# Kernel tuning notes

Hardware: AMD Instinct MI355X
Metric: run time of the kernel (lower is better)

## Reference

```python
import jax, jax.numpy as jnp
import numpy as np

N_CRYST = 256
ATOMS_PER = 64
N_ATOMS = N_CRYST * ATOMS_PER          # 16384
N_EDGES = N_ATOMS * 20                 # 327680 (max_neighbors=20)
HID = 128                              # hidden_dim / emb_size_atom / emb_size_edge
LAT = 256                              # latent_dim
NRAD = 128                             # radial basis size
NBLOCK = 3                             # interaction blocks
MAXZ = 100                             # MAX_ATOMIC_NUM
CUTOFF = 6.0


def lattice_matrix(lengths, angles):
    """CDVAE lattice_params_to_matrix: (B,3),(B,3 deg) -> (B,3,3)."""
    a, b, c = lengths[:, 0], lengths[:, 1], lengths[:, 2]
    al, be, ga = (jnp.deg2rad(angles[:, i]) for i in range(3))
    cos_a, cos_b, cos_g = jnp.cos(al), jnp.cos(be), jnp.cos(ga)
    sin_a, sin_b = jnp.sin(al), jnp.sin(be)
    val = jnp.clip((cos_a * cos_b - cos_g) / (sin_a * sin_b), -1.0, 1.0)
    gs = jnp.arccos(val)  # gamma*
    zero = jnp.zeros_like(a)
    va = jnp.stack([a * sin_b, zero, a * cos_b], -1)
    vb = jnp.stack([-b * sin_a * jnp.cos(gs), b * sin_a * jnp.sin(gs), b * cos_a], -1)
    vc = jnp.stack([zero, zero, c], -1)
    return jnp.stack([va, vb, vc], 1)


def setup_inputs() -> dict:
    key = jax.random.key(0)
    ks = jax.random.split(key, 20)
    p = lambda k, shp: jax.random.normal(k, shp, jnp.float32) * 0.05
    inp = {
        "z": jax.random.normal(ks[0], (N_CRYST, LAT), jnp.float32),
        "pred_frac_coords": jax.random.uniform(ks[1], (N_ATOMS, 3), jnp.float32),
        "pred_atom_types": jax.random.randint(ks[2], (N_ATOMS,), 0, MAXZ),
        "num_atoms": jnp.full((N_CRYST,), ATOMS_PER, jnp.int32),
        "lengths": 5.0 + 5.0 * jax.random.uniform(ks[3], (N_CRYST, 3), jnp.float32),
        "angles": 60.0 + 60.0 * jax.random.uniform(ks[4], (N_CRYST, 3), jnp.float32),
        "edge_index": jax.random.randint(ks[5], (2, N_EDGES), 0, N_ATOMS),
        # learned parameters
        "atom_emb": p(ks[6], (MAXZ, HID)),
        "W_in": p(ks[7], (HID + LAT, HID)), "b_in": jnp.zeros((HID,), jnp.float32),
        "W_rbf": p(ks[8], (NRAD, HID)),
        "W_edge": p(ks[9], (3 * HID, HID)), "b_edge": jnp.zeros((HID,), jnp.float32),
        "W_msg": p(ks[10], (NBLOCK, HID, HID)), "b_msg": jnp.zeros((NBLOCK, HID), jnp.float32),
        "W_gate": p(ks[11], (NBLOCK, HID, HID)),
        "W_upd": p(ks[12], (NBLOCK, HID, HID)), "b_upd": jnp.zeros((NBLOCK, HID), jnp.float32),
        "W_force": p(ks[13], (HID, 1)),
        "W_atom": p(ks[14], (HID, MAXZ)), "b_atom": jnp.zeros((MAXZ,), jnp.float32),
    }
    return inp


def reference(z, pred_frac_coords, pred_atom_types, num_atoms, lengths, angles,
              edge_index, atom_emb, W_in, b_in, W_rbf, W_edge, b_edge,
              W_msg, b_msg, W_gate, W_upd, b_upd, W_force, W_atom, b_atom):
    silu = jax.nn.silu
    batch = jnp.arange(N_ATOMS) // ATOMS_PER  # atom -> crystal (uniform 64 atoms/crystal)

    # fractional -> cartesian using per-crystal lattice
    latt = lattice_matrix(lengths, angles)                       # (B,3,3)
    cart = jnp.einsum("ni,nij->nj", pred_frac_coords, latt[batch])  # (N,3)

    src, dst = edge_index[0], edge_index[1]
    vec = cart[dst] - cart[src]                                   # (E,3)
    d = jnp.linalg.norm(vec, axis=-1) + 1e-8                      # (E,)
    unit = vec / d[:, None]

    # radial basis with smooth cosine envelope
    centers = jnp.linspace(0.0, CUTOFF, NRAD)
    width = CUTOFF / NRAD
    env = 0.5 * (jnp.cos(jnp.pi * jnp.clip(d / CUTOFF, 0.0, 1.0)) + 1.0)
    rbf = jnp.exp(-((d[:, None] - centers) ** 2) / (2.0 * width * width)) * env[:, None]
    rbf_h = rbf @ W_rbf                                           # (E,HID)

    # atom embedding conditioned on latent z (broadcast per crystal)
    h = silu(jnp.concatenate([atom_emb[pred_atom_types], z[batch]], -1) @ W_in + b_in)

    # edge embedding
    m = silu(jnp.concatenate([h[src], h[dst], rbf_h], -1) @ W_edge + b_edge)  # (E,HID)

    # interaction blocks: edge message update, rbf gating, scatter to atoms
    for i in range(NBLOCK):
        m2 = silu(m @ W_msg[i] + b_msg[i]) * (rbf_h @ W_gate[i])
        agg = jax.ops.segment_sum(m2, dst, num_segments=N_ATOMS)  # (N,HID)
        h = h + silu(agg @ W_upd[i] + b_upd[i])
        m = m + m2

    # per-edge force scalar -> cartesian coord diff per atom
    f_edge = (m @ W_force) * unit                                 # (E,3)
    pred_cart_coord_diff = jax.ops.segment_sum(f_edge, dst, num_segments=N_ATOMS)

    pred_atom_types_out = h @ W_atom + b_atom                     # (N,MAXZ)
    return (pred_cart_coord_diff, pred_atom_types_out)
```

## Files before the change

kernel.cpp:

```cpp
#include <hip/hip_runtime.h>
#include <hip/hip_bf16.h>

#define N_CRYST 256
#define ATOMS_PER 64
#define N_ATOMS (N_CRYST * ATOMS_PER)
#define N_EDGES (N_ATOMS * 20)
#define HID 128
#define LAT 256
#define NRAD 128
#define NBLOCK 3
#define MAXZ 100
#define CUTOFF 6.0f
#define PI_F 3.14159265358979323846f
#define ETILE 64
#define TABN 2048

typedef unsigned short ushort_t;
typedef unsigned char uchar_t;
typedef unsigned long long ull_t;
typedef __attribute__((ext_vector_type(8))) short short8;
typedef __attribute__((ext_vector_type(4))) float f32x4;

__device__ __forceinline__ float fexp2(float x) {
    float r; asm("v_exp_f32 %0, %1" : "=v"(r) : "v"(x)); return r;
}
__device__ __forceinline__ float frcp(float x) {
    float r; asm("v_rcp_f32 %0, %1" : "=v"(r) : "v"(x)); return r;
}
__device__ __forceinline__ float silu(float x) {
    return x * frcp(1.0f + fexp2(x * -1.44269504f));
}

__device__ __forceinline__ ushort_t f2bf(float v) {
    unsigned int u = __float_as_uint(v);
    return (ushort_t)((u + 0x7FFF + ((u >> 16) & 1)) >> 16);
}
__device__ __forceinline__ float bf2f(ushort_t u) {
    return __uint_as_float((unsigned int)u << 16);
}
__device__ __forceinline__ unsigned int pkbf(float lo, float hi) {
    unsigned int r;
    asm("v_cvt_pk_bf16_f32 %0, %1, %2" : "=v"(r) : "v"(lo), "v"(hi));
    return r;
}

__device__ __forceinline__ f32x4 MFMA(short8 a, short8 b, f32x4 c) {
    return __builtin_amdgcn_mfma_f32_16x16x32_bf16(a, b, c, 0, 0, 0);
}

__device__ __forceinline__ int swz(int row, int k) {
    return (row * 256 + k * 2) ^ ((row & 7) << 4);
}

__device__ __forceinline__ short8 ldB(const ushort_t* W, int col, int K, int k) {
    return *reinterpret_cast<const short8*>(W + (size_t)col * K + k);
}

__global__ void k_init(float* __restrict__ out, float* __restrict__ agg,
                       int* __restrict__ cnt) {
    int i = blockIdx.x * blockDim.x + threadIdx.x;
    if (i < N_ATOMS * 3) out[i] = 0.0f;
    if (i < N_ATOMS) cnt[i] = 0;
    if (i < NBLOCK * N_ATOMS * HID) agg[i] = 0.0f;
}

__global__ void k_hist(const int* __restrict__ edge_index, int* __restrict__ cnt) {
    int e = blockIdx.x * blockDim.x + threadIdx.x;
    if (e < N_EDGES) atomicAdd(&cnt[edge_index[N_EDGES + e]], 1);
}

__global__ void k_scan(const int* __restrict__ cnt, int* __restrict__ cursor) {
    __shared__ int partial[256];
    int t = threadIdx.x;
    int base = t * (N_ATOMS / 256);
    int s = 0;
    for (int j = 0; j < N_ATOMS / 256; j++) s += cnt[base + j];
    partial[t] = s;
    __syncthreads();
    if (t == 0) {
        int run = 0;
        for (int i = 0; i < 256; i++) { int v = partial[i]; partial[i] = run; run += v; }
    }
    __syncthreads();
    int run = partial[t];
    for (int j = 0; j < N_ATOMS / 256; j++) {
        cursor[base + j] = run;
        run += cnt[base + j];
    }
}

__global__ void k_scatter(const int* __restrict__ edge_index,
                          int* __restrict__ cursor, int* __restrict__ perm) {
    int e = blockIdx.x * blockDim.x + threadIdx.x;
    if (e < N_EDGES) {
        int pos = atomicAdd(&cursor[edge_index[N_EDGES + e]], 1);
        perm[pos] = e;
    }
}

__global__ void k_latt(const float* __restrict__ lengths,
                       const float* __restrict__ angles,
                       float* __restrict__ latt) {
    int c = blockIdx.x * blockDim.x + threadIdx.x;
    if (c >= N_CRYST) return;
    float a  = lengths[c * 3 + 0];
    float b  = lengths[c * 3 + 1];
    float cc = lengths[c * 3 + 2];
    float al = angles[c * 3 + 0] * (PI_F / 180.0f);
    float be = angles[c * 3 + 1] * (PI_F / 180.0f);
    float ga = angles[c * 3 + 2] * (PI_F / 180.0f);
    float cos_a = cosf(al), cos_b = cosf(be), cos_g = cosf(ga);
    float sin_a = sinf(al), sin_b = sinf(be);
    float val = (cos_a * cos_b - cos_g) / (sin_a * sin_b);
    val = fminf(1.0f, fmaxf(-1.0f, val));
    float gs = acosf(val);
    float* L = latt + c * 9;
    L[0] = a * sin_b;              L[1] = 0.0f;                  L[2] = a * cos_b;
    L[3] = -b * sin_a * cosf(gs);  L[4] = b * sin_a * sinf(gs);  L[5] = b * cos_a;
    L[6] = 0.0f;                   L[7] = 0.0f;                  L[8] = cc;
}

__global__ void k_cart(const float* __restrict__ frac,
                       const float* __restrict__ latt,
                       float* __restrict__ cart) {
    int n = blockIdx.x * blockDim.x + threadIdx.x;
    if (n >= N_ATOMS) return;
    int b = n / ATOMS_PER;
    const float* L = latt + b * 9;
    float f0 = frac[n * 3 + 0], f1 = frac[n * 3 + 1], f2 = frac[n * 3 + 2];
    cart[n * 3 + 0] = f0 * L[0] + f1 * L[3] + f2 * L[6];
    cart[n * 3 + 1] = f0 * L[1] + f1 * L[4] + f2 * L[7];
    cart[n * 3 + 2] = f0 * L[2] + f1 * L[5] + f2 * L[8];
}

__global__ void k_tab(const float* __restrict__ W_rbf, float* __restrict__ T) {
    int j = blockIdx.x;
    int c = threadIdx.x;
    __shared__ float rbf[NRAD];
    float d = (float)j * (CUTOFF / TABN);
    const float inv2w2 = 1.0f / (2.0f * (CUTOFF / NRAD) * (CUTOFF / NRAD));
    const float cstep = CUTOFF / (NRAD - 1);
    float x = fminf(1.0f, d * (1.0f / CUTOFF));
    float env = 0.5f * (cosf(PI_F * x) + 1.0f);
    float diff = d - (float)c * cstep;
    rbf[c] = expf(-diff * diff * inv2w2) * env;
    __syncthreads();
    float acc = 0.0f;
#pragma unroll 8
    for (int k = 0; k < NRAD; k++) acc += rbf[k] * W_rbf[k * HID + c];
    T[j * HID + c] = acc;
}

__global__ void k_prep(const float* __restrict__ W_edge,
                       const float* __restrict__ W_msg,
                       const float* __restrict__ W_gate,
                       const float* __restrict__ W_upd,
                       const float* __restrict__ W_atom,
                       ushort_t* __restrict__ Wt_edge,
                       ushort_t* __restrict__ Wt_msg,
                       ushort_t* __restrict__ Wt_gate,
                       ushort_t* __restrict__ Wt_upd,
                       ushort_t* __restrict__ Wt_atom) {
    int i = blockIdx.x * blockDim.x + threadIdx.x;
    if (i < 128 * 384) {
        int c = i / 384, k = i % 384;
        Wt_edge[(size_t)c * 384 + k] = f2bf(W_edge[k * 128 + c]);
    }
    if (i < 3 * 128 * 128) {
        int blk = i >> 14, r = i & 16383;
        int c = r >> 7, k = r & 127;
        Wt_msg[blk * 16384 + c * 128 + k]  = f2bf(W_msg[blk * 16384 + k * 128 + c]);
        Wt_gate[blk * 16384 + c * 128 + k] = f2bf(W_gate[blk * 16384 + k * 128 + c]);
        Wt_upd[blk * 16384 + c * 128 + k]  = f2bf(W_upd[blk * 16384 + k * 128 + c]);
    }
    if (i < 128 * 128) {
        int c = i >> 7, k = i & 127;
        Wt_atom[c * 128 + k] = (c < MAXZ) ? f2bf(W_atom[k * MAXZ + c]) : (ushort_t)0;
    }
}

__global__ void k_embW(const float* __restrict__ atom_emb,
                       const float* __restrict__ W_in,
                       const float* __restrict__ b_in,
                       float* __restrict__ embW) {
    int zi = blockIdx.x;
    int c = threadIdx.x;
    __shared__ float row[HID];
    row[c] = atom_emb[zi * HID + c];
    __syncthreads();
    float acc = b_in[c];
#pragma unroll 8
    for (int k = 0; k < HID; k++) acc += row[k] * W_in[k * HID + c];
    embW[zi * HID + c] = acc;
}

__global__ void k_zW(const float* __restrict__ z,
                     const float* __restrict__ W_in,
                     float* __restrict__ zW) {
    int b = blockIdx.x;
    int c = threadIdx.x;
    __shared__ float row[LAT];
    row[c]       = z[b * LAT + c];
    row[128 + c] = z[b * LAT + 128 + c];
    __syncthreads();
    float acc = 0.f;
#pragma unroll 8
    for (int k = 0; k < LAT; k++) acc += row[k] * W_in[(HID + k) * HID + c];
    zW[b * HID + c] = acc;
}

__global__ void k_h2(const int* __restrict__ types,
                     const float* __restrict__ embW,
                     const float* __restrict__ zW,
                     ushort_t* __restrict__ h_bf) {
    int idx = blockIdx.x * 256 + threadIdx.x;
    int n = idx >> 7, c = idx & 127;
    float v = embW[types[n] * HID + c] + zW[(n >> 6) * HID + c];
    h_bf[idx] = f2bf(silu(v));
}

__global__ __launch_bounds__(512, 4)
void k_edges(const int* __restrict__ perm,
             const int* __restrict__ edge_index,
             const float* __restrict__ cart,
             const float* __restrict__ T,
             const ushort_t* __restrict__ h_bf,
             const ushort_t* __restrict__ Wt_edge,
             const float* __restrict__ b_edge,
             const ushort_t* __restrict__ Wt_msg,
             const float* __restrict__ b_msg,
             const ushort_t* __restrict__ Wt_gate,
             const float* __restrict__ W_force,
             float* __restrict__ agg,
             float* __restrict__ outF)
{
    __shared__ ushort_t R2[ETILE * HID];
    __shared__ ushort_t HSR3[ETILE * HID];
    __shared__ ushort_t HD[ETILE * HID];
    __shared__ int   sm_dst[ETILE];
    __shared__ float sm_unit[ETILE][3];
    __shared__ float sm_d[ETILE];
    __shared__ float sm_f[ETILE];
    __shared__ uchar_t sm_runid8[ETILE];
    __shared__ int   sm_slotdst[ETILE];
    __shared__ int   sm_nruns;
    ushort_t* M2T = HD;

    const int t    = threadIdx.x;
    const int lane = t & 63;
    const int wave = t >> 6;
    const int l15  = lane & 15;
    const int g4   = lane >> 4;
    const int lk8  = 8 * g4;
    const int colw = wave * 16;
    const int e0   = blockIdx.x * ETILE;

    const int laneA = l15 * 256 + ((lk8 * 2) ^ ((l15 & 7) << 4));
    const int colM  = colw + l15;
    int woff[4];
#pragma unroll
    for (int r = 0; r < 4; r++) {
        int row = g4 * 4 + r;
        woff[r] = row * 256 + ((colM * 2) ^ ((row & 7) << 4));
    }

    if (t < ETILE) {
        int e = t;
        int eid = perm[e0 + e];
        int s = edge_index[eid];
        int d = edge_index[N_EDGES + eid];
        sm_dst[e] = d;
        float vx = cart[d * 3 + 0] - cart[s * 3 + 0];
        float vy = cart[d * 3 + 1] - cart[s * 3 + 1];
        float vz = cart[d * 3 + 2] - cart[s * 3 + 2];
        float dist = sqrtf(vx * vx + vy * vy + vz * vz) + 1e-8f;
        sm_d[e] = dist;
        float di = 1.0f / dist;
        sm_unit[e][0] = vx * di; sm_unit[e][1] = vy * di; sm_unit[e][2] = vz * di;
        sm_f[e] = 0.0f;
    }
    __syncthreads();

    short8 hs[2], hd[2];
    int stoff[2];
#pragma unroll
    for (int p = 0; p < 2; p++) {
        int u   = p * 512 + t;
        int row = u >> 4;
        int seg = u & 15;
        int eid = perm[e0 + row];
        int s = edge_index[eid];
        int d = edge_index[N_EDGES + eid];
        hs[p] = *reinterpret_cast<const short8*>(h_bf + (size_t)s * HID + seg * 8);
        hd[p] = *reinterpret_cast<const short8*>(h_bf + (size_t)d * HID + seg * 8);
        stoff[p] = swz(row, seg * 8);
    }

    if (wave == 0) {
        int e = lane;
        int d = sm_dst[e];
        int prev = (e == 0) ? -1 : sm_dst[e - 1];
        ull_t mask = __ballot(d != prev);
        int rid = __popcll(mask & ((2ull << e) - 1)) - 1;
        sm_runid8[e] = (uchar_t)rid;
        if (d != prev) sm_slotdst[rid] = d;
        if (e == 0) sm_nruns = __popcll(mask);
    }

    {
#pragma unroll
        for (int it = 0; it < 4; it++) {
            int u = it * 512 + t;
            int e = u >> 5;
            int p = u & 31;
            float idxf = sm_d[e] * (TABN / CUTOFF);
            idxf = fminf(idxf, (float)TABN);
            int j = (int)idxf;
            float fr = idxf - (float)j;
            f32x4 lo = *reinterpret_cast<const f32x4*>(T + (size_t)j * HID + 4 * p);
            f32x4 hi = *reinterpret_cast<const f32x4*>(T + (size_t)(j + 1) * HID + 4 * p);
            float v0 = lo[0] + fr * (hi[0] - lo[0]);
            float v1 = lo[1] + fr * (hi[1] - lo[1]);
            float v2 = lo[2] + fr * (hi[2] - lo[2]);
            float v3 = lo[3] + fr * (hi[3] - lo[3]);
            unsigned int pk0 = pkbf(v0, v1);
            unsigned int pk1 = pkbf(v2, v3);
            int off = (e * 256 + 8 * p) ^ ((e & 7) << 4);
            *reinterpret_cast<unsigned int*>(reinterpret_cast<char*>(R2) + off)     = pk0;
            *reinterpret_cast<unsigned int*>(reinterpret_cast<char*>(R2) + off + 4) = pk1;
        }
#pragma unroll
        for (int p = 0; p < 2; p++) {
            *reinterpret_cast<short8*>(reinterpret_cast<char*>(HSR3) + stoff[p]) = hs[p];
            *reinterpret_cast<short8*>(reinterpret_cast<char*>(HD)   + stoff[p]) = hd[p];
        }
    }
    __syncthreads();

    float m_acc[4][4];
    {
        f32x4 am[4];
#pragma unroll
        for (int at = 0; at < 4; at++) am[at] = (f32x4){0.f, 0.f, 0.f, 0.f};
        const ushort_t* segp[3] = {HSR3, HD, R2};
#pragma unroll
        for (int seg = 0; seg < 3; seg++) {
#pragma unroll
            for (int ks = 0; ks < 4; ks++) {
                int kg = seg * 128 + ks * 32 + lk8;
                short8 B0 = ldB(Wt_edge, colM, 384, kg);
                int lA = laneA ^ (ks * 64);
#pragma unroll
                for (int at = 0; at < 4; at++) {
                    short8 A = *reinterpret_cast<const short8*>(
                        reinterpret_cast<const char*>(segp[seg]) + (lA + at * 4096));
                    am[at] = MFMA(A, B0, am[at]);
                }
            }
        }
        float be0 = b_edge[colM];
#pragma unroll
        for (int at = 0; at < 4; at++)
#pragma unroll
            for (int r = 0; r < 4; r++)
                m_acc[at][r] = silu(am[at][r] + be0);
    }
    __syncthreads();

#pragma unroll
    for (int at = 0; at < 4; at++)
#pragma unroll
        for (int r = 0; r < 4; r++)
            *reinterpret_cast<ushort_t*>(reinterpret_cast<char*>(HSR3) +
                (woff[r] + at * 4096)) = f2bf(m_acc[at][r]);
    __syncthreads();

    for (int i = 0; i < NBLOCK; i++) {
        const ushort_t* Wm = Wt_msg  + i * 16384;
        const ushort_t* Wg = Wt_gate + i * 16384;
        float* aggp = agg + (size_t)i * N_ATOMS * HID;
        {
            float bm = b_msg[i * HID + colM];
            f32x4 am_[4], ag_[4];
#pragma unroll
            for (int at = 0; at < 4; at++) {
                am_[at] = (f32x4){0.f, 0.f, 0.f, 0.f};
                ag_[at] = (f32x4){0.f, 0.f, 0.f, 0.f};
            }
#pragma unroll
            for (int ks = 0; ks < 4; ks++) {
                short8 Bm = ldB(Wm, colM, 128, ks * 32 + lk8);
                short8 Bg = ldB(Wg, colM, 128, ks * 32 + lk8);
                int lA = laneA ^ (ks * 64);
#pragma unroll
                for (int at = 0; at < 4; at++) {
                    short8 Am = *reinterpret_cast<const short8*>(
                        reinterpret_cast<const char*>(HSR3) + (lA + at * 4096));
                    short8 Ag = *reinterpret_cast<const short8*>(
                        reinterpret_cast<const char*>(R2) + (lA + at * 4096));
                    am_[at] = MFMA(Am, Bm, am_[at]);
                    ag_[at] = MFMA(Ag, Bg, ag_[at]);
                }
            }
#pragma unroll
            for (int at = 0; at < 4; at++) {
                float m2v[4];
#pragma unroll
                for (int r = 0; r < 4; r++) {
                    float m2 = silu(am_[at][r] + bm) * ag_[at][r];
                    m2v[r] = m2;
                    m_acc[at][r] += m2;
                }
                unsigned int plo = pkbf(m2v[0], m2v[1]);
                unsigned int phi = pkbf(m2v[2], m2v[3]);
                ull_t pk = ((ull_t)phi << 32) | plo;
                int addr = (colM * 128 + (at * 16 + g4 * 4) * 2) ^ ((colM & 7) << 4);
                *reinterpret_cast<ull_t*>(reinterpret_cast<char*>(M2T) + addr) = pk;
            }
        }
        __syncthreads();

        {
            int nruns = sm_nruns;
            short8 Bm2[2];
#pragma unroll
            for (int ks = 0; ks < 2; ks++) {
                int addr = (colM * 128 + (ks * 32 + lk8) * 2) ^ ((colM & 7) << 4);
                Bm2[ks] = *reinterpret_cast<const short8*>(
                    reinterpret_cast<const char*>(M2T) + addr);
            }
            for (int rt = 0; rt * 16 < nruns; rt++) {
                int tv = l15 + rt * 16;
                short8 SA[2];
#pragma unroll
                for (int ks = 0; ks < 2; ks++) {
                    ull_t rid8 = *reinterpret_cast<const ull_t*>(sm_runid8 + ks * 32 + lk8);
                    unsigned int rlo = (unsigned int)rid8;
                    unsigned int rhi = (unsigned int)(rid8 >> 32);
                    union { unsigned int u[4]; short8 s8; } sb;
#pragma unroll
                    for (int q = 0; q < 2; q++) {
                        unsigned int rr = q ? rhi : rlo;
                        unsigned int w0 = 0, w1 = 0;
                        if ((int)((rr >>  0) & 255) == tv) w0 |= 0x3F80u;
                        if ((int)((rr >>  8) & 255) == tv) w0 |= 0x3F800000u;
                        if ((int)((rr >> 16) & 255) == tv) w1 |= 0x3F80u;
                        if ((int)((rr >> 24) & 255) == tv) w1 |= 0x3F800000u;
                        sb.u[q * 2]     = w0;
                        sb.u[q * 2 + 1] = w1;
                    }
                    SA[ks] = sb.s8;
                }
                f32x4 acc0 = {0.f, 0.f, 0.f, 0.f};
                acc0 = MFMA(SA[0], Bm2[0], acc0);
                acc0 = MFMA(SA[1], Bm2[1], acc0);
#pragma unroll
                for (int r = 0; r < 4; r++) {
                    int run = rt * 16 + g4 * 4 + r;
                    if (run < nruns) {
                        int d = sm_slotdst[run];
                        atomicAdd(&aggp[(size_t)d * HID + colM], acc0[r]);
                    }
                }
            }
        }

        if (i < NBLOCK - 1) {
#pragma unroll
            for (int at = 0; at < 4; at++)
#pragma unroll
                for (int r = 0; r < 4; r++)
                    *reinterpret_cast<ushort_t*>(reinterpret_cast<char*>(HSR3) +
                        (woff[r] + at * 4096)) = f2bf(m_acc[at][r]);
        }
        __syncthreads();
    }

    {
        float wf0 = W_force[colM];
#pragma unroll
        for (int at = 0; at < 4; at++)
#pragma unroll
            for (int r = 0; r < 4; r++) {
                float part = m_acc[at][r] * wf0;
                part += __shfl_xor(part, 1, 64);
                part += __shfl_xor(part, 2, 64);
                part += __shfl_xor(part, 4, 64);
                part += __shfl_xor(part, 8, 64);
                if (l15 == 0)
                    atomicAdd(&sm_f[at * 16 + g4 * 4 + r], part);
            }
        __syncthreads();
        if (t < ETILE) {
            int e = t;
            int d = sm_dst[e];
            if (e == 0 || sm_dst[e - 1] != d) {
                float fx = 0.f, fy = 0.f, fz = 0.f;
                int j = e;
                do {
                    float f = sm_f[j];
                    fx += f * sm_unit[j][0];
                    fy += f * sm_unit[j][1];
                    fz += f * sm_unit[j][2];
                    j++;
                } while (j < ETILE && sm_dst[j] == d);
                atomicAdd(&outF[d * 3 + 0], fx);
                atomicAdd(&outF[d * 3 + 1], fy);
                atomicAdd(&outF[d * 3 + 2], fz);
            }
        }
    }
}

__global__ __launch_bounds__(256)
void k_atom2(const float* __restrict__ agg,
             const ushort_t* __restrict__ Wt_upd,
             const float* __restrict__ b_upd,
             const ushort_t* __restrict__ Wt_atom,
             const float* __restrict__ b_atom,
             const ushort_t* __restrict__ h_bf,
             float* __restrict__ out) {
    __shared__ ushort_t RA[64 * HID];

    const int t    = threadIdx.x;
    const int lane = t & 63;
    const int wave = t >> 6;
    const int l15  = lane & 15;
    const int lk8  = 8 * (lane >> 4);
    const int colw = wave * 32;
    const int n0   = blockIdx.x * 64;

    const int laneA = l15 * 256 + ((lk8 * 2) ^ ((l15 & 7) << 4));
    int woff[2][4];
#pragma unroll
    for (int nt = 0; nt < 2; nt++)
#pragma unroll
        for (int r = 0; r < 4; r++) {
            int row = (lane >> 4) * 4 + r;
            woff[nt][r] = row * 256 + (((colw + nt * 16 + l15) * 2) ^ ((row & 7) << 4));
        }

    float h_acc[4][2][4];
#pragma unroll
    for (int at = 0; at < 4; at++)
#pragma unroll
        for (int nt = 0; nt < 2; nt++)
#pragma unroll
            for (int r = 0; r < 4; r++) {
                int row = at * 16 + (lane >> 4) * 4 + r;
                h_acc[at][nt][r] = bf2f(h_bf[(size_t)(n0 + row) * HID + colw + nt * 16 + l15]);
            }

    for (int i = 0; i < NBLOCK; i++) {
        const float* ap = agg + (size_t)i * N_ATOMS * HID + (size_t)n0 * HID;
#pragma unroll
        for (int it = 0; it < 8; it++) {
            int u = it * 256 + t;
            int row = u >> 5, p = u & 31;
            f32x4 v = *reinterpret_cast<const f32x4*>(ap + (size_t)row * HID + 4 * p);
            unsigned int pk0 = pkbf(v[0], v[1]);
            unsigned int pk1 = pkbf(v[2], v[3]);
            int off = (row * 256 + 8 * p) ^ ((row & 7) << 4);
            *reinterpret_cast<unsigned int*>(reinterpret_cast<char*>(RA) + off)     = pk0;
            *reinterpret_cast<unsigned int*>(reinterpret_cast<char*>(RA) + off + 4) = pk1;
        }
        __syncthreads();

        const ushort_t* Wu = Wt_upd + i * 16384;
        float bu0 = b_upd[i * HID + colw + l15];
        float bu1 = b_upd[i * HID + colw + 16 + l15];
        f32x4 am[4][2];
#pragma unroll
        for (int at = 0; at < 4; at++)
#pragma unroll
            for (int nt = 0; nt < 2; nt++)
                am[at][nt] = (f32x4){0.f, 0.f, 0.f, 0.f};
#pragma unroll
        for (int ks = 0; ks < 4; ks++) {
            short8 B0 = ldB(Wu, colw + l15,      128, ks * 32 + lk8);
            short8 B1 = ldB(Wu, colw + 16 + l15, 128, ks * 32 + lk8);
            int lA = laneA ^ (ks * 64);
#pragma unroll
            for (int at = 0; at < 4; at++) {
                short8 A = *reinterpret_cast<const short8*>(
                    reinterpret_cast<const char*>(RA) + (lA + at * 4096));
                am[at][0] = MFMA(A, B0, am[at][0]);
                am[at][1] = MFMA(A, B1, am[at][1]);
            }
        }
#pragma unroll
        for (int at = 0; at < 4; at++)
#pragma unroll
            for (int r = 0; r < 4; r++) {
                h_acc[at][0][r] += silu(am[at][0][r] + bu0);
                h_acc[at][1][r] += silu(am[at][1][r] + bu1);
            }
        __syncthreads();
    }

#pragma unroll
    for (int at = 0; at < 4; at++)
#pragma unroll
        for (int nt = 0; nt < 2; nt++)
#pragma unroll
            for (int r = 0; r < 4; r++)
                *reinterpret_cast<ushort_t*>(reinterpret_cast<char*>(RA) +
                    (woff[nt][r] + at * 4096)) = f2bf(h_acc[at][nt][r]);
    __syncthreads();

    {
        f32x4 am[4][2];
#pragma unroll
        for (int at = 0; at < 4; at++)
#pragma unroll
            for (int nt = 0; nt < 2; nt++)
                am[at][nt] = (f32x4){0.f, 0.f, 0.f, 0.f};
#pragma unroll
        for (int ks = 0; ks < 4; ks++) {
            short8 B0 = ldB(Wt_atom, colw + l15,      128, ks * 32 + lk8);
            short8 B1 = ldB(Wt_atom, colw + 16 + l15, 128, ks * 32 + lk8);
            int lA = laneA ^ (ks * 64);
#pragma unroll
            for (int at = 0; at < 4; at++) {
                short8 A = *reinterpret_cast<const short8*>(
                    reinterpret_cast<const char*>(RA) + (lA + at * 4096));
                am[at][0] = MFMA(A, B0, am[at][0]);
                am[at][1] = MFMA(A, B1, am[at][1]);
            }
        }
        int col0 = colw + l15;
        int col1 = colw + 16 + l15;
        float ba0 = (col0 < MAXZ) ? b_atom[col0] : 0.f;
        float ba1 = (col1 < MAXZ) ? b_atom[col1] : 0.f;
#pragma unroll
        for (int at = 0; at < 4; at++)
#pragma unroll
            for (int r = 0; r < 4; r++) {
                int row = n0 + at * 16 + (lane >> 4) * 4 + r;
                if (col0 < MAXZ)
                    out[(size_t)N_ATOMS * 3 + (size_t)row * MAXZ + col0] = am[at][0][r] + ba0;
                if (col1 < MAXZ)
                    out[(size_t)N_ATOMS * 3 + (size_t)row * MAXZ + col1] = am[at][1][r] + ba1;
            }
    }
}

extern "C" void kernel_launch(void* const* d_in, const int* in_sizes, int n_in,
                              void* d_out, int out_size, void* d_ws, size_t ws_size,
                              hipStream_t stream) {
    const float* z         = (const float*)d_in[0];
    const float* frac      = (const float*)d_in[1];
    const int*   types     = (const int*)d_in[2];
    const float* lengths   = (const float*)d_in[4];
    const float* angles    = (const float*)d_in[5];
    const int*   edge_idx  = (const int*)d_in[6];
    const float* atom_emb  = (const float*)d_in[7];
    const float* W_in      = (const float*)d_in[8];
    const float* b_in      = (const float*)d_in[9];
    const float* W_rbf     = (const float*)d_in[10];
    const float* W_edge    = (const float*)d_in[11];
    const float* b_edge    = (const float*)d_in[12];
    const float* W_msg     = (const float*)d_in[13];
    const float* b_msg     = (const float*)d_in[14];
    const float* W_gate    = (const float*)d_in[15];
    const float* W_upd     = (const float*)d_in[16];
    const float* b_upd     = (const float*)d_in[17];
    const float* W_force   = (const float*)d_in[18];
    const float* W_atom    = (const float*)d_in[19];
    const float* b_atom    = (const float*)d_in[20];

    float* out = (float*)d_out;

    float* ws = (float*)d_ws;
    size_t off = 0;
    float* latt = ws + off; off += N_CRYST * 9;
    float* cart = ws + off; off += (size_t)N_ATOMS * 3;
    float* agg  = ws + off; off += (size_t)NBLOCK * N_ATOMS * HID;
    float* embW = ws + off; off += MAXZ * HID;
    float* zW   = ws + off; off += N_CRYST * HID;
    float* T    = ws + off; off += (size_t)(TABN + 2) * HID;
    int* cnt    = (int*)(ws + off); off += N_ATOMS;
    int* cursor = (int*)(ws + off); off += N_ATOMS;
    int* perm   = (int*)(ws + off); off += N_EDGES;
    off = (off + 7) & ~(size_t)7;
    ushort_t* ub = (ushort_t*)(ws + off);
    size_t uoff = 0;
    ushort_t* h_bf    = ub + uoff; uoff += (size_t)N_ATOMS * HID;
    ushort_t* Wt_edge = ub + uoff; uoff += 128 * 384;
    ushort_t* Wt_msg  = ub + uoff; uoff += 3 * 128 * 128;
    ushort_t* Wt_gate = ub + uoff; uoff += 3 * 128 * 128;
    ushort_t* Wt_upd  = ub + uoff; uoff += 3 * 128 * 128;
    ushort_t* Wt_atom = ub + uoff; uoff += 128 * 128;

    k_init<<<(NBLOCK * N_ATOMS * HID + 255) / 256, 256, 0, stream>>>(out, agg, cnt);

    k_hist<<<(N_EDGES + 255) / 256, 256, 0, stream>>>(edge_idx, cnt);
    k_scan<<<1, 256, 0, stream>>>(cnt, cursor);
    k_scatter<<<(N_EDGES + 255) / 256, 256, 0, stream>>>(edge_idx, cursor, perm);

    k_latt<<<1, 256, 0, stream>>>(lengths, angles, latt);
    k_cart<<<(N_ATOMS + 255) / 256, 256, 0, stream>>>(frac, latt, cart);
    k_tab<<<TABN + 2, HID, 0, stream>>>(W_rbf, T);
    k_prep<<<192, 256, 0, stream>>>(W_edge, W_msg, W_gate, W_upd, W_atom,
                                    Wt_edge, Wt_msg, Wt_gate, Wt_upd, Wt_atom);

    k_embW<<<MAXZ, HID, 0, stream>>>(atom_emb, W_in, b_in, embW);
    k_zW<<<N_CRYST, HID, 0, stream>>>(z, W_in, zW);
    k_h2<<<(N_ATOMS * HID) / 256, 256, 0, stream>>>(types, embW, zW, h_bf);

    k_edges<<<N_EDGES / ETILE, 512, 0, stream>>>(perm, edge_idx, cart, T, h_bf,
                                                 Wt_edge, b_edge,
                                                 Wt_msg, b_msg, Wt_gate, W_force,
                                                 agg, out);

    k_atom2<<<N_ATOMS / 64, 256, 0, stream>>>(agg, Wt_upd, b_upd, Wt_atom, b_atom,
                                              h_bf, out);
}
```

Baseline: 393.5 us.

## Merge preprocessing kernels into two multi-role launches and halve atom tile

The histogram, lattice/cartesian, RBF table, weight transpose, embW and zW kernels are folded into one launch that picks its role from block-index ranges. The lattice matrix is now computed inline per atom, so its workspace buffer goes away. The edge scatter and the h embedding kernels are merged into a second launch. Separately, the atom update kernel now handles 32 atoms per block instead of 64, doubling the block count to fill more CUs. The goal is to remove launch overhead and serialization between small kernels. The cost is recomputing trig per atom and less weight reuse per block in the atom kernel.

```diff
diff --git a/kernel.cpp b/kernel.cpp
--- a/kernel.cpp
+++ b/kernel.cpp
@@ -64,11 +64,6 @@
     if (i < NBLOCK * N_ATOMS * HID) agg[i] = 0.0f;
 }
 
-__global__ void k_hist(const int* __restrict__ edge_index, int* __restrict__ cnt) {
-    int e = blockIdx.x * blockDim.x + threadIdx.x;
-    if (e < N_EDGES) atomicAdd(&cnt[edge_index[N_EDGES + e]], 1);
-}
-
 __global__ void k_scan(const int* __restrict__ cnt, int* __restrict__ cursor) {
     __shared__ int partial[256];
     int t = threadIdx.x;
@@ -89,134 +84,120 @@
     }
 }
 
-__global__ void k_scatter(const int* __restrict__ edge_index,
-                          int* __restrict__ cursor, int* __restrict__ perm) {
-    int e = blockIdx.x * blockDim.x + threadIdx.x;
-    if (e < N_EDGES) {
+#define F0_HIST 1280
+#define F0_CART (F0_HIST + 64)
+#define F0_TAB  (F0_CART + 1025)
+#define F0_PREP (F0_TAB + 192)
+#define F0_EMBW (F0_PREP + 50)
+#define F0_ZW   (F0_EMBW + 128)
+__global__ void k_fuse0(const int* __restrict__ edge_index, int* __restrict__ cnt,
+                        const float* __restrict__ lengths, const float* __restrict__ angles,
+                        const float* __restrict__ frac, float* __restrict__ cart,
+                        const float* __restrict__ W_rbf, float* __restrict__ T,
+                        const float* __restrict__ W_edge, const float* __restrict__ W_msg,
+                        const float* __restrict__ W_gate, const float* __restrict__ W_upd,
+                        const float* __restrict__ W_atom,
+                        ushort_t* __restrict__ Wt_edge, ushort_t* __restrict__ Wt_msg,
+                        ushort_t* __restrict__ Wt_gate, ushort_t* __restrict__ Wt_upd,
+                        ushort_t* __restrict__ Wt_atom,
+                        const float* __restrict__ atom_emb, const float* __restrict__ W_in,
+                        const float* __restrict__ b_in, float* __restrict__ embW,
+                        const float* __restrict__ z, float* __restrict__ zW) {
+    __shared__ float sh[512];
+    int b = blockIdx.x, t = threadIdx.x;
+    if (b < F0_HIST) {
+        int e = b * 256 + t;
+        atomicAdd(&cnt[edge_index[N_EDGES + e]], 1);
+    } else if (b < F0_CART) {
+        int n = (b - F0_HIST) * 256 + t;
+        int c = n >> 6;
+        float a  = lengths[c * 3 + 0];
+        float bb = lengths[c * 3 + 1];
+        float cc = lengths[c * 3 + 2];
+        float al = angles[c * 3 + 0] * (PI_F / 180.0f);
+        float be = angles[c * 3 + 1] * (PI_F / 180.0f);
+        float ga = angles[c * 3 + 2] * (PI_F / 180.0f);
+        float cos_a = cosf(al), cos_b = cosf(be), cos_g = cosf(ga);
+        float sin_a = sinf(al), sin_b = sinf(be);
+        float val = (cos_a * cos_b - cos_g) / (sin_a * sin_b);
+        val = fminf(1.0f, fmaxf(-1.0f, val));
+        float gs = acosf(val);
+        float L0 = a * sin_b, L2 = a * cos_b;
+        float L3 = -bb * sin_a * cosf(gs), L4 = bb * sin_a * sinf(gs), L5 = bb * cos_a;
+        float f0 = frac[n * 3 + 0], f1 = frac[n * 3 + 1], f2 = frac[n * 3 + 2];
+        cart[n * 3 + 0] = f0 * L0 + f1 * L3;
+        cart[n * 3 + 1] = f1 * L4;
+        cart[n * 3 + 2] = f0 * L2 + f1 * L5 + f2 * cc;
+    } else if (b < F0_TAB) {
+        int half = t >> 7, c = t & 127;
+        int j = (b - F0_CART) * 2 + half;
+        float d = (float)j * (CUTOFF / TABN);
+        const float inv2w2 = 1.0f / (2.0f * (CUTOFF / NRAD) * (CUTOFF / NRAD));
+        const float cstep = CUTOFF / (NRAD - 1);
+        float x = fminf(1.0f, d * (1.0f / CUTOFF));
+        float env = 0.5f * (cosf(PI_F * x) + 1.0f);
+        float diff = d - (float)c * cstep;
+        sh[half * 128 + c] = expf(-diff * diff * inv2w2) * env;
+        __syncthreads();
+        float acc = 0.0f;
+#pragma unroll 8
+        for (int k = 0; k < NRAD; k++) acc += sh[half * 128 + k] * W_rbf[k * HID + c];
+        T[(size_t)j * HID + c] = acc;
+    } else if (b < F0_PREP) {
+        int i = (b - F0_TAB) * 256 + t;
+        {
+            int c = i / 384, k = i % 384;
+            Wt_edge[(size_t)c * 384 + k] = f2bf(W_edge[k * 128 + c]);
+        }
+        {
+            int blk = i >> 14, r = i & 16383;
+            int c = r >> 7, k = r & 127;
+            Wt_msg[blk * 16384 + c * 128 + k]  = f2bf(W_msg[blk * 16384 + k * 128 + c]);
+            Wt_gate[blk * 16384 + c * 128 + k] = f2bf(W_gate[blk * 16384 + k * 128 + c]);
+            Wt_upd[blk * 16384 + c * 128 + k]  = f2bf(W_upd[blk * 16384 + k * 128 + c]);
+        }
+        if (i < 128 * 128) {
+            int c = i >> 7, k = i & 127;
+            Wt_atom[c * 128 + k] = (c < MAXZ) ? f2bf(W_atom[k * MAXZ + c]) : (ushort_t)0;
+        }
+    } else if (b < F0_EMBW) {
+        int half = t >> 7, c = t & 127;
+        int zi = (b - F0_PREP) * 2 + half;
+        sh[half * 128 + c] = atom_emb[zi * HID + c];
+        __syncthreads();
+        float acc = b_in[c];
+#pragma unroll 8
+        for (int k = 0; k < HID; k++) acc += sh[half * 128 + k] * W_in[k * HID + c];
+        embW[zi * HID + c] = acc;
+    } else {
+        int half = t >> 7, c = t & 127;
+        int bc = (b - F0_EMBW) * 2 + half;
+        sh[half * 256 + c]       = z[bc * LAT + c];
+        sh[half * 256 + 128 + c] = z[bc * LAT + 128 + c];
+        __syncthreads();
+        float acc = 0.f;
+#pragma unroll 8
+        for (int k = 0; k < LAT; k++) acc += sh[half * 256 + k] * W_in[(HID + k) * HID + c];
+        zW[bc * HID + c] = acc;
+    }
+}
+
+__global__ void k_fuse1(const int* __restrict__ edge_index,
+                        int* __restrict__ cursor, int* __restrict__ perm,
+                        const int* __restrict__ types,
+                        const float* __restrict__ embW, const float* __restrict__ zW,
+                        ushort_t* __restrict__ h_bf) {
+    int b = blockIdx.x, t = threadIdx.x;
+    if (b < 1280) {
+        int e = b * 256 + t;
         int pos = atomicAdd(&cursor[edge_index[N_EDGES + e]], 1);
         perm[pos] = e;
-    }
-}
-
-__global__ void k_latt(const float* __restrict__ lengths,
-                       const float* __restrict__ angles,
-                       float* __restrict__ latt) {
-    int c = blockIdx.x * blockDim.x + threadIdx.x;
-    if (c >= N_CRYST) return;
-    float a  = lengths[c * 3 + 0];
-    float b  = lengths[c * 3 + 1];
-    float cc = lengths[c * 3 + 2];
-    float al = angles[c * 3 + 0] * (PI_F / 180.0f);
-    float be = angles[c * 3 + 1] * (PI_F / 180.0f);
-    float ga = angles[c * 3 + 2] * (PI_F / 180.0f);
-    float cos_a = cosf(al), cos_b = cosf(be), cos_g = cosf(ga);
-    float sin_a = sinf(al), sin_b = sinf(be);
-    float val = (cos_a * cos_b - cos_g) / (sin_a * sin_b);
-    val = fminf(1.0f, fmaxf(-1.0f, val));
-    float gs = acosf(val);
-    float* L = latt + c * 9;
-    L[0] = a * sin_b;              L[1] = 0.0f;                  L[2] = a * cos_b;
-    L[3] = -b * sin_a * cosf(gs);  L[4] = b * sin_a * sinf(gs);  L[5] = b * cos_a;
-    L[6] = 0.0f;                   L[7] = 0.0f;                  L[8] = cc;
-}
-
-__global__ void k_cart(const float* __restrict__ frac,
-                       const float* __restrict__ latt,
-                       float* __restrict__ cart) {
-    int n = blockIdx.x * blockDim.x + threadIdx.x;
-    if (n >= N_ATOMS) return;
-    int b = n / ATOMS_PER;
-    const float* L = latt + b * 9;
-    float f0 = frac[n * 3 + 0], f1 = frac[n * 3 + 1], f2 = frac[n * 3 + 2];
-    cart[n * 3 + 0] = f0 * L[0] + f1 * L[3] + f2 * L[6];
-    cart[n * 3 + 1] = f0 * L[1] + f1 * L[4] + f2 * L[7];
-    cart[n * 3 + 2] = f0 * L[2] + f1 * L[5] + f2 * L[8];
-}
-
-__global__ void k_tab(const float* __restrict__ W_rbf, float* __restrict__ T) {
-    int j = blockIdx.x;
-    int c = threadIdx.x;
-    __shared__ float rbf[NRAD];
-    float d = (float)j * (CUTOFF / TABN);
-    const float inv2w2 = 1.0f / (2.0f * (CUTOFF / NRAD) * (CUTOFF / NRAD));
-    const float cstep = CUTOFF / (NRAD - 1);
-    float x = fminf(1.0f, d * (1.0f / CUTOFF));
-    float env = 0.5f * (cosf(PI_F * x) + 1.0f);
-    float diff = d - (float)c * cstep;
-    rbf[c] = expf(-diff * diff * inv2w2) * env;
-    __syncthreads();
-    float acc = 0.0f;
-#pragma unroll 8
-    for (int k = 0; k < NRAD; k++) acc += rbf[k] * W_rbf[k * HID + c];
-    T[j * HID + c] = acc;
-}
-
-__global__ void k_prep(const float* __restrict__ W_edge,
-                       const float* __restrict__ W_msg,
-                       const float* __restrict__ W_gate,
-                       const float* __restrict__ W_upd,
-                       const float* __restrict__ W_atom,
-                       ushort_t* __restrict__ Wt_edge,
-                       ushort_t* __restrict__ Wt_msg,
-                       ushort_t* __restrict__ Wt_gate,
-                       ushort_t* __restrict__ Wt_upd,
-                       ushort_t* __restrict__ Wt_atom) {
-    int i = blockIdx.x * blockDim.x + threadIdx.x;
-    if (i < 128 * 384) {
-        int c = i / 384, k = i % 384;
-        Wt_edge[(size_t)c * 384 + k] = f2bf(W_edge[k * 128 + c]);
-    }
-    if (i < 3 * 128 * 128) {
-        int blk = i >> 14, r = i & 16383;
-        int c = r >> 7, k = r & 127;
-        Wt_msg[blk * 16384 + c * 128 + k]  = f2bf(W_msg[blk * 16384 + k * 128 + c]);
-        Wt_gate[blk * 16384 + c * 128 + k] = f2bf(W_gate[blk * 16384 + k * 128 + c]);
-        Wt_upd[blk * 16384 + c * 128 + k]  = f2bf(W_upd[blk * 16384 + k * 128 + c]);
-    }
-    if (i < 128 * 128) {
-        int c = i >> 7, k = i & 127;
-        Wt_atom[c * 128 + k] = (c < MAXZ) ? f2bf(W_atom[k * MAXZ + c]) : (ushort_t)0;
-    }
-}
-
-__global__ void k_embW(const float* __restrict__ atom_emb,
-                       const float* __restrict__ W_in,
-                       const float* __restrict__ b_in,
-                       float* __restrict__ embW) {
-    int zi = blockIdx.x;
-    int c = threadIdx.x;
-    __shared__ float row[HID];
-    row[c] = atom_emb[zi * HID + c];
-    __syncthreads();
-    float acc = b_in[c];
-#pragma unroll 8
-    for (int k = 0; k < HID; k++) acc += row[k] * W_in[k * HID + c];
-    embW[zi * HID + c] = acc;
-}
-
-__global__ void k_zW(const float* __restrict__ z,
-                     const float* __restrict__ W_in,
-                     float* __restrict__ zW) {
-    int b = blockIdx.x;
-    int c = threadIdx.x;
-    __shared__ float row[LAT];
-    row[c]       = z[b * LAT + c];
-    row[128 + c] = z[b * LAT + 128 + c];
-    __syncthreads();
-    float acc = 0.f;
-#pragma unroll 8
-    for (int k = 0; k < LAT; k++) acc += row[k] * W_in[(HID + k) * HID + c];
-    zW[b * HID + c] = acc;
-}
-
-__global__ void k_h2(const int* __restrict__ types,
-                     const float* __restrict__ embW,
-                     const float* __restrict__ zW,
-                     ushort_t* __restrict__ h_bf) {
-    int idx = blockIdx.x * 256 + threadIdx.x;
-    int n = idx >> 7, c = idx & 127;
-    float v = embW[types[n] * HID + c] + zW[(n >> 6) * HID + c];
-    h_bf[idx] = f2bf(silu(v));
+    } else {
+        int idx = (b - 1280) * 256 + t;
+        int n = idx >> 7, c = idx & 127;
+        float v = embW[types[n] * HID + c] + zW[(n >> 6) * HID + c];
+        h_bf[idx] = f2bf(silu(v));
+    }
 }
 
 __global__ __launch_bounds__(512, 4)
@@ -520,7 +501,7 @@
              const float* __restrict__ b_atom,
              const ushort_t* __restrict__ h_bf,
              float* __restrict__ out) {
-    __shared__ ushort_t RA[64 * HID];
+    __shared__ ushort_t RA[32 * HID];
 
     const int t    = threadIdx.x;
     const int lane = t & 63;
@@ -528,7 +509,7 @@
     const int l15  = lane & 15;
     const int lk8  = 8 * (lane >> 4);
     const int colw = wave * 32;
-    const int n0   = blockIdx.x * 64;
+    const int n0   = blockIdx.x * 32;
 
     const int laneA = l15 * 256 + ((lk8 * 2) ^ ((l15 & 7) << 4));
     int woff[2][4];
@@ -540,9 +521,9 @@
             woff[nt][r] = row * 256 + (((colw + nt * 16 + l15) * 2) ^ ((row & 7) << 4));
         }
 
-    float h_acc[4][2][4];
-#pragma unroll
-    for (int at = 0; at < 4; at++)
+    float h_acc[2][2][4];
+#pragma unroll
+    for (int at = 0; at < 2; at++)
 #pragma unroll
         for (int nt = 0; nt < 2; nt++)
 #pragma unroll
@@ -554,7 +535,7 @@
     for (int i = 0; i < NBLOCK; i++) {
         const float* ap = agg + (size_t)i * N_ATOMS * HID + (size_t)n0 * HID;
 #pragma unroll
-        for (int it = 0; it < 8; it++) {
+        for (int it = 0; it < 4; it++) {
             int u = it * 256 + t;
             int row = u >> 5, p = u & 31;
             f32x4 v = *reinterpret_cast<const f32x4*>(ap + (size_t)row * HID + 4 * p);
@@ -569,9 +550,9 @@
         const ushort_t* Wu = Wt_upd + i * 16384;
         float bu0 = b_upd[i * HID + colw + l15];
         float bu1 = b_upd[i * HID + colw + 16 + l15];
-        f32x4 am[4][2];
-#pragma unroll
-        for (int at = 0; at < 4; at++)
+        f32x4 am[2][2];
+#pragma unroll
+        for (int at = 0; at < 2; at++)
 #pragma unroll
             for (int nt = 0; nt < 2; nt++)
                 am[at][nt] = (f32x4){0.f, 0.f, 0.f, 0.f};
@@ -581,7 +562,7 @@
             short8 B1 = ldB(Wu, colw + 16 + l15, 128, ks * 32 + lk8);
             int lA = laneA ^ (ks * 64);
 #pragma unroll
-            for (int at = 0; at < 4; at++) {
+            for (int at = 0; at < 2; at++) {
                 short8 A = *reinterpret_cast<const short8*>(
                     reinterpret_cast<const char*>(RA) + (lA + at * 4096));
                 am[at][0] = MFMA(A, B0, am[at][0]);
@@ -589,7 +570,7 @@
             }
         }
 #pragma unroll
-        for (int at = 0; at < 4; at++)
+        for (int at = 0; at < 2; at++)
 #pragma unroll
             for (int r = 0; r < 4; r++) {
                 h_acc[at][0][r] += silu(am[at][0][r] + bu0);
@@ -599,7 +580,7 @@
     }
 
 #pragma unroll
-    for (int at = 0; at < 4; at++)
+    for (int at = 0; at < 2; at++)
 #pragma unroll
         for (int nt = 0; nt < 2; nt++)
 #pragma unroll
@@ -609,9 +590,9 @@
     __syncthreads();
 
     {
-        f32x4 am[4][2];
-#pragma unroll
-        for (int at = 0; at < 4; at++)
+        f32x4 am[2][2];
+#pragma unroll
+        for (int at = 0; at < 2; at++)
 #pragma unroll
             for (int nt = 0; nt < 2; nt++)
                 am[at][nt] = (f32x4){0.f, 0.f, 0.f, 0.f};
@@ -621,7 +602,7 @@
             short8 B1 = ldB(Wt_atom, colw + 16 + l15, 128, ks * 32 + lk8);
             int lA = laneA ^ (ks * 64);
 #pragma unroll
-            for (int at = 0; at < 4; at++) {
+            for (int at = 0; at < 2; at++) {
                 short8 A = *reinterpret_cast<const short8*>(
                     reinterpret_cast<const char*>(RA) + (lA + at * 4096));
                 am[at][0] = MFMA(A, B0, am[at][0]);
@@ -633,7 +614,7 @@
         float ba0 = (col0 < MAXZ) ? b_atom[col0] : 0.f;
         float ba1 = (col1 < MAXZ) ? b_atom[col1] : 0.f;
 #pragma unroll
-        for (int at = 0; at < 4; at++)
+        for (int at = 0; at < 2; at++)
 #pragma unroll
             for (int r = 0; r < 4; r++) {
                 int row = n0 + at * 16 + (lane >> 4) * 4 + r;
@@ -673,7 +654,6 @@
 
     float* ws = (float*)d_ws;
     size_t off = 0;
-    float* latt = ws + off; off += N_CRYST * 9;
     float* cart = ws + off; off += (size_t)N_ATOMS * 3;
     float* agg  = ws + off; off += (size_t)NBLOCK * N_ATOMS * HID;
     float* embW = ws + off; off += MAXZ * HID;
@@ -694,25 +674,22 @@
 
     k_init<<<(NBLOCK * N_ATOMS * HID + 255) / 256, 256, 0, stream>>>(out, agg, cnt);
 
-    k_hist<<<(N_EDGES + 255) / 256, 256, 0, stream>>>(edge_idx, cnt);
+    k_fuse0<<<F0_ZW, 256, 0, stream>>>(edge_idx, cnt, lengths, angles, frac, cart,
+                                       W_rbf, T,
+                                       W_edge, W_msg, W_gate, W_upd, W_atom,
+                                       Wt_edge, Wt_msg, Wt_gate, Wt_upd, Wt_atom,
+                                       atom_emb, W_in, b_in, embW, z, zW);
+
     k_scan<<<1, 256, 0, stream>>>(cnt, cursor);
-    k_scatter<<<(N_EDGES + 255) / 256, 256, 0, stream>>>(edge_idx, cursor, perm);
-
-    k_latt<<<1, 256, 0, stream>>>(lengths, angles, latt);
-    k_cart<<<(N_ATOMS + 255) / 256, 256, 0, stream>>>(frac, latt, cart);
-    k_tab<<<TABN + 2, HID, 0, stream>>>(W_rbf, T);
-    k_prep<<<192, 256, 0, stream>>>(W_edge, W_msg, W_gate, W_upd, W_atom,
-                                    Wt_edge, Wt_msg, Wt_gate, Wt_upd, Wt_atom);
-
-    k_embW<<<MAXZ, HID, 0, stream>>>(atom_emb, W_in, b_in, embW);
-    k_zW<<<N_CRYST, HID, 0, stream>>>(z, W_in, zW);
-    k_h2<<<(N_ATOMS * HID) / 256, 256, 0, stream>>>(types, embW, zW, h_bf);
+
+    k_fuse1<<<1280 + (N_ATOMS * HID) / 256, 256, 0, stream>>>(edge_idx, cursor, perm,
+                                                              types, embW, zW, h_bf);
 
     k_edges<<<N_EDGES / ETILE, 512, 0, stream>>>(perm, edge_idx, cart, T, h_bf,
                                                  Wt_edge, b_edge,
                                                  Wt_msg, b_msg, Wt_gate, W_force,
                                                  agg, out);
 
-    k_atom2<<<N_ATOMS / 64, 256, 0, stream>>>(agg, Wt_upd, b_upd, Wt_atom, b_atom,
+    k_atom2<<<N_ATOMS / 32, 256, 0, stream>>>(agg, Wt_upd, b_upd, Wt_atom, b_atom,
                                               h_bf, out);
 }
```

After: 366.9 us. -6.7%, faster.
